# Kernel optimization log

Measured on AMD Instinct MI355X. Metric: run time of the kernel, lower is better.

The kernel has to match this reference:

```python
import jax, jax.numpy as jnp
import numpy as np

B, L, C, K = 8, 4096, 256, 3
PAD = 1  # (K-1)//2, required so offset/mask conv preserves length L


def conv1d(x, w, b, padding):
    # x: (B, C, L), w: (O, C, K), b: (O,)
    y = jax.lax.conv_general_dilated(
        x, w, window_strides=(1,), padding=[(padding, padding)],
        dimension_numbers=('NCH', 'OIH', 'NCH'))
    return y + b[None, :, None]


def setup_inputs() -> dict:
    key = jax.random.key(0)
    ks = jax.random.split(key, 5)
    fan = 1.0 / np.sqrt(C * K)
    return {
        'x': jax.random.normal(ks[0], (B, L, C), dtype=jnp.float32),
        'w_off': jax.random.uniform(ks[1], (K, C, K), jnp.float32, -fan, fan),
        'b_off': jax.random.uniform(ks[2], (K,), jnp.float32, -fan, fan),
        'w_mask': jax.random.uniform(ks[3], (K, C, K), jnp.float32, -fan, fan),
        'b_mask': jax.random.uniform(ks[4], (K,), jnp.float32, -fan, fan),
    }


def reference(x, w_off, b_off, w_mask, b_mask):
    b, l, c = x.shape
    xt = jnp.transpose(x, (0, 2, 1))                      # (B, C, L)
    offset = conv1d(xt, w_off, b_off, PAD)                # (B, K, L)
    mask = jax.nn.sigmoid(conv1d(xt, w_mask, b_mask, PAD))  # (B, K, L)

    # pos = l + offset, clamped; offset is shared across channels.
    i = jnp.arange(l, dtype=x.dtype)[None, None, :]       # (1, 1, L)
    pos = jnp.clip(i + offset, 0.0, l - 1)                # (B, K, L)
    fl = jnp.floor(pos).astype(jnp.int32)                 # (B, K, L)
    ce = jnp.minimum(fl + 1, l - 1)
    alpha = pos - fl.astype(x.dtype)                      # (B, K, L)

    # gather per batch: (C, L)[:, (K, L)] -> (C, K, L)
    gather = jax.vmap(lambda xb, idx: xb[:, idx])
    x_floor = gather(xt, fl)                              # (B, C, K, L)
    x_ceil = gather(xt, ce)                               # (B, C, K, L)
    a = alpha[:, None, :, :]
    sampled = x_floor * (1.0 - a) + x_ceil * a            # (B, C, K, L)

    out = (sampled * mask[:, None, :, :]).sum(axis=2)     # (B, C, L)
    # Faithful to torch: output.view(B, L, out_channels) is a raw reshape
    # of the contiguous (B, C, L) buffer, NOT a transpose.
    return out.reshape(b, l, c)
```

## Files before the change

kernel.cpp:

```cpp
#include <hip/hip_runtime.h>
#include <math.h>

#define B_  8
#define L_  4096
#define C_  256
#define TL  32

template<int CTRL, int RM>
__device__ __forceinline__ float dpp_add(float v) {
    int mv = __builtin_amdgcn_update_dpp(0, __float_as_int(v), CTRL, RM, 0xf, true);
    return v + __int_as_float(mv);
}
__device__ __forceinline__ float wave_sum_hi(float v) {
    v = dpp_add<0xB1, 0xf>(v);
    v = dpp_add<0x4E, 0xf>(v);
    v = dpp_add<0x141, 0xf>(v);
    v = dpp_add<0x140, 0xf>(v);
    v = dpp_add<0x142, 0xa>(v);
    v = dpp_add<0x143, 0xc>(v);
    return v;
}
__device__ __forceinline__ float bcast63(float v) {
    return __int_as_float(__builtin_amdgcn_readlane(__float_as_int(v), 63));
}

__global__ __launch_bounds__(512, 2)
void dconv1d_kernel(const float* __restrict__ x,
                    const float* __restrict__ w_off,
                    const float* __restrict__ b_off,
                    const float* __restrict__ w_mask,
                    const float* __restrict__ b_mask,
                    float* __restrict__ out) {
    __shared__ float s_tile[TL * C_];

    const int tid  = threadIdx.x;
    const int lane = tid & 63;
    const int wv   = tid >> 6;
    const int wgid = blockIdx.x;
    const int b    = wgid & 7;
    const int l0   = (wgid >> 3) * TL;
    const float* __restrict__ xb = x + (size_t)b * L_ * C_;

    const float bo0 = b_off[0],  bo1 = b_off[1],  bo2 = b_off[2];
    const float bm0 = b_mask[0], bm1 = b_mask[1], bm2 = b_mask[2];

    const int c4  = lane << 2;
    const int lb4 = l0 + wv * 4;

    float4 xrow[6];
    #pragma unroll
    for (int rr = 0; rr < 6; ++rr) {
        const int row = lb4 - 1 + rr;
        if (row >= 0 && row < L_)
            xrow[rr] = *reinterpret_cast<const float4*>(
                xb + (size_t)row * C_ + c4);
        else
            xrow[rr] = make_float4(0.f, 0.f, 0.f, 0.f);
    }

    float sums_off[4][3];
    #pragma unroll
    for (int o = 0; o < 3; ++o) {
        const float4* wp = reinterpret_cast<const float4*>(
            w_off + o * (C_ * 3) + lane * 12);
        const float4 w0 = wp[0], w1 = wp[1], w2 = wp[2];
        float acc[4] = {0.f, 0.f, 0.f, 0.f};
        #pragma unroll
        for (int rr = 0; rr < 6; ++rr) {
            #pragma unroll
            for (int tt = 0; tt < 3; ++tt) {
                const int i = rr - tt;
                if (i >= 0 && i < 4) {
                    const float wt0 = (tt==0)?w0.x:((tt==1)?w0.y:w0.z);
                    const float wt1 = (tt==0)?w0.w:((tt==1)?w1.x:w1.y);
                    const float wt2 = (tt==0)?w1.z:((tt==1)?w1.w:w2.x);
                    const float wt3 = (tt==0)?w2.y:((tt==1)?w2.z:w2.w);
                    acc[i] += xrow[rr].x * wt0 + xrow[rr].y * wt1
                            + xrow[rr].z * wt2 + xrow[rr].w * wt3;
                }
            }
        }
        #pragma unroll
        for (int i = 0; i < 4; ++i)
            sums_off[i][o] = bcast63(wave_sum_hi(acc[i]));
    }

    float4 gxf[4][3], gxc[4][3];
    float  alp[4][3];
    #pragma unroll
    for (int i = 0; i < 4; ++i) {
        const int l = lb4 + i;
        #pragma unroll
        for (int k = 0; k < 3; ++k) {
            const float bo = (k == 0) ? bo0 : ((k == 1) ? bo1 : bo2);
            const float off = sums_off[i][k] + bo;
            const float pos = fminf(fmaxf((float)l + off, 0.0f), (float)(L_ - 1));
            const float flf = floorf(pos);
            const int   fl  = (int)flf;
            const int   ce  = min(fl + 1, L_ - 1);
            alp[i][k] = pos - flf;
            gxf[i][k] = *reinterpret_cast<const float4*>(
                xb + (size_t)fl * C_ + c4);
            gxc[i][k] = *reinterpret_cast<const float4*>(
                xb + (size_t)ce * C_ + c4);
        }
    }

    float sums_msk[4][3];
    #pragma unroll
    for (int o = 0; o < 3; ++o) {
        const float4* wp = reinterpret_cast<const float4*>(
            w_mask + o * (C_ * 3) + lane * 12);
        const float4 w0 = wp[0], w1 = wp[1], w2 = wp[2];
        float acc[4] = {0.f, 0.f, 0.f, 0.f};
        #pragma unroll
        for (int rr = 0; rr < 6; ++rr) {
            #pragma unroll
            for (int tt = 0; tt < 3; ++tt) {
                const int i = rr - tt;
                if (i >= 0 && i < 4) {
                    const float wt0 = (tt==0)?w0.x:((tt==1)?w0.y:w0.z);
                    const float wt1 = (tt==0)?w0.w:((tt==1)?w1.x:w1.y);
                    const float wt2 = (tt==0)?w1.z:((tt==1)?w1.w:w2.x);
                    const float wt3 = (tt==0)?w2.y:((tt==1)?w2.z:w2.w);
                    acc[i] += xrow[rr].x * wt0 + xrow[rr].y * wt1
                            + xrow[rr].z * wt2 + xrow[rr].w * wt3;
                }
            }
        }
        #pragma unroll
        for (int i = 0; i < 4; ++i)
            sums_msk[i][o] = bcast63(wave_sum_hi(acc[i]));
    }

    #pragma unroll
    for (int i = 0; i < 4; ++i) {
        const int ll = wv * 4 + i;
        float4 v = make_float4(0.f, 0.f, 0.f, 0.f);
        #pragma unroll
        for (int k = 0; k < 3; ++k) {
            const float bm = (k == 0) ? bm0 : ((k == 1) ? bm1 : bm2);
            const float m  = 1.0f / (1.0f + __expf(-(sums_msk[i][k] + bm)));
            const float a  = alp[i][k];
            const float wf = m * (1.0f - a);
            const float wc = m * a;
            const float4 xf = gxf[i][k];
            const float4 xc = gxc[i][k];
            v.x += wf * xf.x + wc * xc.x;
            v.y += wf * xf.y + wc * xc.y;
            v.z += wf * xf.z + wc * xc.z;
            v.w += wf * xf.w + wc * xc.w;
        }
        const int gr = lane ^ (ll & 15);
        *reinterpret_cast<float4*>(&s_tile[ll * C_ + (gr << 2)]) = v;
    }
    __syncthreads();

    {
        const int lw = tid & 31;
        const int q0 = tid >> 5;
        #pragma unroll
        for (int s = 0; s < 4; ++s) {
            const int q  = q0 + (s << 4);
            const int gr = q ^ (lw & 15);
            const float4 v = *reinterpret_cast<const float4*>(
                &s_tile[lw * C_ + (gr << 2)]);
            const size_t ob = ((size_t)b * C_ + (q << 2)) * L_ + l0 + lw;
            out[ob]          = v.x;
            out[ob + L_]     = v.y;
            out[ob + 2 * L_] = v.z;
            out[ob + 3 * L_] = v.w;
        }
    }
}

extern "C" void kernel_launch(void* const* d_in, const int* in_sizes, int n_in,
                              void* d_out, int out_size, void* d_ws, size_t ws_size,
                              hipStream_t stream) {
    const float* x      = (const float*)d_in[0];
    const float* w_off  = (const float*)d_in[1];
    const float* b_off  = (const float*)d_in[2];
    const float* w_mask = (const float*)d_in[3];
    const float* b_mask = (const float*)d_in[4];
    float* out = (float*)d_out;

    dconv1d_kernel<<<(L_ / TL) * B_, 512, 0, stream>>>(
        x, w_off, b_off, w_mask, b_mask, out);
}
```

Before: 26.82 us.

## Double sequence tile to 64 rows, eight per wave, with staged gathers

Raises the tile from 32 to 64 sequence positions per block, so each wave computes eight output rows from ten loaded halo rows instead of four from six. This cuts the relative halo reload and the weight loads per output. The gather loads are split into two batches around the mask convolution, and the shared-memory swizzle and store pattern are redone so that 64 lanes write 64 contiguous positions. In exchange it uses more registers and a 64 KB shared tile, which may lower occupancy below the declared two blocks per CU, and it halves the grid to 512 blocks.

```diff
diff --git a/kernel.cpp b/kernel.cpp
--- a/kernel.cpp
+++ b/kernel.cpp
@@ -4,7 +4,7 @@
 #define B_  8
 #define L_  4096
 #define C_  256
-#define TL  32
+#define TL  64
 
 template<int CTRL, int RM>
 __device__ __forceinline__ float dpp_add(float v) {
@@ -45,12 +45,12 @@
     const float bm0 = b_mask[0], bm1 = b_mask[1], bm2 = b_mask[2];
 
     const int c4  = lane << 2;
-    const int lb4 = l0 + wv * 4;
-
-    float4 xrow[6];
-    #pragma unroll
-    for (int rr = 0; rr < 6; ++rr) {
-        const int row = lb4 - 1 + rr;
+    const int lb8 = l0 + wv * 8;
+
+    float4 xrow[10];
+    #pragma unroll
+    for (int rr = 0; rr < 10; ++rr) {
+        const int row = lb8 - 1 + rr;
         if (row >= 0 && row < L_)
             xrow[rr] = *reinterpret_cast<const float4*>(
                 xb + (size_t)row * C_ + c4);
@@ -58,19 +58,19 @@
             xrow[rr] = make_float4(0.f, 0.f, 0.f, 0.f);
     }
 
-    float sums_off[4][3];
+    float sums_off[8][3];
     #pragma unroll
     for (int o = 0; o < 3; ++o) {
         const float4* wp = reinterpret_cast<const float4*>(
             w_off + o * (C_ * 3) + lane * 12);
         const float4 w0 = wp[0], w1 = wp[1], w2 = wp[2];
-        float acc[4] = {0.f, 0.f, 0.f, 0.f};
-        #pragma unroll
-        for (int rr = 0; rr < 6; ++rr) {
+        float acc[8] = {0.f,0.f,0.f,0.f,0.f,0.f,0.f,0.f};
+        #pragma unroll
+        for (int rr = 0; rr < 10; ++rr) {
             #pragma unroll
             for (int tt = 0; tt < 3; ++tt) {
                 const int i = rr - tt;
-                if (i >= 0 && i < 4) {
+                if (i >= 0 && i < 8) {
                     const float wt0 = (tt==0)?w0.x:((tt==1)?w0.y:w0.z);
                     const float wt1 = (tt==0)?w0.w:((tt==1)?w1.x:w1.y);
                     const float wt2 = (tt==0)?w1.z:((tt==1)?w1.w:w2.x);
@@ -81,15 +81,15 @@
             }
         }
         #pragma unroll
-        for (int i = 0; i < 4; ++i)
+        for (int i = 0; i < 8; ++i)
             sums_off[i][o] = bcast63(wave_sum_hi(acc[i]));
     }
 
-    float4 gxf[4][3], gxc[4][3];
-    float  alp[4][3];
-    #pragma unroll
-    for (int i = 0; i < 4; ++i) {
-        const int l = lb4 + i;
+    float4 gxf0[4][3], gxc0[4][3];
+    float  alp0[4][3];
+    #pragma unroll
+    for (int i = 0; i < 4; ++i) {
+        const int l = lb8 + i;
         #pragma unroll
         for (int k = 0; k < 3; ++k) {
             const float bo = (k == 0) ? bo0 : ((k == 1) ? bo1 : bo2);
@@ -98,27 +98,27 @@
             const float flf = floorf(pos);
             const int   fl  = (int)flf;
             const int   ce  = min(fl + 1, L_ - 1);
-            alp[i][k] = pos - flf;
-            gxf[i][k] = *reinterpret_cast<const float4*>(
+            alp0[i][k] = pos - flf;
+            gxf0[i][k] = *reinterpret_cast<const float4*>(
                 xb + (size_t)fl * C_ + c4);
-            gxc[i][k] = *reinterpret_cast<const float4*>(
+            gxc0[i][k] = *reinterpret_cast<const float4*>(
                 xb + (size_t)ce * C_ + c4);
         }
     }
 
-    float sums_msk[4][3];
+    float sums_msk[8][3];
     #pragma unroll
     for (int o = 0; o < 3; ++o) {
         const float4* wp = reinterpret_cast<const float4*>(
             w_mask + o * (C_ * 3) + lane * 12);
         const float4 w0 = wp[0], w1 = wp[1], w2 = wp[2];
-        float acc[4] = {0.f, 0.f, 0.f, 0.f};
-        #pragma unroll
-        for (int rr = 0; rr < 6; ++rr) {
+        float acc[8] = {0.f,0.f,0.f,0.f,0.f,0.f,0.f,0.f};
+        #pragma unroll
+        for (int rr = 0; rr < 10; ++rr) {
             #pragma unroll
             for (int tt = 0; tt < 3; ++tt) {
                 const int i = rr - tt;
-                if (i >= 0 && i < 4) {
+                if (i >= 0 && i < 8) {
                     const float wt0 = (tt==0)?w0.x:((tt==1)?w0.y:w0.z);
                     const float wt1 = (tt==0)?w0.w:((tt==1)?w1.x:w1.y);
                     const float wt2 = (tt==0)?w1.z:((tt==1)?w1.w:w2.x);
@@ -129,40 +129,78 @@
             }
         }
         #pragma unroll
-        for (int i = 0; i < 4; ++i)
+        for (int i = 0; i < 8; ++i)
             sums_msk[i][o] = bcast63(wave_sum_hi(acc[i]));
     }
 
-    #pragma unroll
-    for (int i = 0; i < 4; ++i) {
-        const int ll = wv * 4 + i;
+    float4 gxf1[4][3], gxc1[4][3];
+    float  alp1[4][3];
+    #pragma unroll
+    for (int i = 0; i < 4; ++i) {
+        const int l = lb8 + 4 + i;
+        #pragma unroll
+        for (int k = 0; k < 3; ++k) {
+            const float bo = (k == 0) ? bo0 : ((k == 1) ? bo1 : bo2);
+            const float off = sums_off[4 + i][k] + bo;
+            const float pos = fminf(fmaxf((float)l + off, 0.0f), (float)(L_ - 1));
+            const float flf = floorf(pos);
+            const int   fl  = (int)flf;
+            const int   ce  = min(fl + 1, L_ - 1);
+            alp1[i][k] = pos - flf;
+            gxf1[i][k] = *reinterpret_cast<const float4*>(
+                xb + (size_t)fl * C_ + c4);
+            gxc1[i][k] = *reinterpret_cast<const float4*>(
+                xb + (size_t)ce * C_ + c4);
+        }
+    }
+
+    #pragma unroll
+    for (int i = 0; i < 4; ++i) {
+        const int ll = wv * 8 + i;
         float4 v = make_float4(0.f, 0.f, 0.f, 0.f);
         #pragma unroll
         for (int k = 0; k < 3; ++k) {
             const float bm = (k == 0) ? bm0 : ((k == 1) ? bm1 : bm2);
             const float m  = 1.0f / (1.0f + __expf(-(sums_msk[i][k] + bm)));
-            const float a  = alp[i][k];
+            const float a  = alp0[i][k];
             const float wf = m * (1.0f - a);
             const float wc = m * a;
-            const float4 xf = gxf[i][k];
-            const float4 xc = gxc[i][k];
-            v.x += wf * xf.x + wc * xc.x;
-            v.y += wf * xf.y + wc * xc.y;
-            v.z += wf * xf.z + wc * xc.z;
-            v.w += wf * xf.w + wc * xc.w;
-        }
-        const int gr = lane ^ (ll & 15);
-        *reinterpret_cast<float4*>(&s_tile[ll * C_ + (gr << 2)]) = v;
+            v.x += wf * gxf0[i][k].x + wc * gxc0[i][k].x;
+            v.y += wf * gxf0[i][k].y + wc * gxc0[i][k].y;
+            v.z += wf * gxf0[i][k].z + wc * gxc0[i][k].z;
+            v.w += wf * gxf0[i][k].w + wc * gxc0[i][k].w;
+        }
+        *reinterpret_cast<float4*>(
+            &s_tile[ll * C_ + ((lane ^ ll) << 2)]) = v;
+    }
+
+    #pragma unroll
+    for (int i = 0; i < 4; ++i) {
+        const int ll = wv * 8 + 4 + i;
+        float4 v = make_float4(0.f, 0.f, 0.f, 0.f);
+        #pragma unroll
+        for (int k = 0; k < 3; ++k) {
+            const float bm = (k == 0) ? bm0 : ((k == 1) ? bm1 : bm2);
+            const float m  = 1.0f / (1.0f + __expf(-(sums_msk[4 + i][k] + bm)));
+            const float a  = alp1[i][k];
+            const float wf = m * (1.0f - a);
+            const float wc = m * a;
+            v.x += wf * gxf1[i][k].x + wc * gxc1[i][k].x;
+            v.y += wf * gxf1[i][k].y + wc * gxc1[i][k].y;
+            v.z += wf * gxf1[i][k].z + wc * gxc1[i][k].z;
+            v.w += wf * gxf1[i][k].w + wc * gxc1[i][k].w;
+        }
+        *reinterpret_cast<float4*>(
+            &s_tile[ll * C_ + ((lane ^ ll) << 2)]) = v;
     }
     __syncthreads();
 
     {
-        const int lw = tid & 31;
-        const int q0 = tid >> 5;
-        #pragma unroll
-        for (int s = 0; s < 4; ++s) {
-            const int q  = q0 + (s << 4);
-            const int gr = q ^ (lw & 15);
+        const int lw = lane;
+        #pragma unroll
+        for (int s = 0; s < 8; ++s) {
+            const int q  = wv + (s << 3);
+            const int gr = q ^ lw;
             const float4 v = *reinterpret_cast<const float4*>(
                 &s_tile[lw * C_ + (gr << 2)]);
             const size_t ob = ((size_t)b * C_ + (q << 2)) * L_ + l0 + lw;
```

Result: slower. 33.79 us (+26.0%).
